# Performance work log

Measured on AMD Instinct MI355X. Metric: run time of the kernel, lower is better.

Reference implementation:

```python
import jax, jax.numpy as jnp
import numpy as np

B = 1024
S_OUT, S_IN, D_IN = 30, 17, 3
H = 4
DKQ_I, DV_I, HID_I, OUT_I = 6, 8, 256, 64
DKQ_O, DV_O, HID_O = 64, 64, 1024
OUT_O = 36 * S_OUT  # 1080


def _mha(x, wq, bq, wk, bk, wv, bv, dkq):
    """Vectorized multi-head self-attention over all heads at once.
    x: [..., P, d_in]; wq/wk: [H, d_in, dkq]; wv: [H, d_in, dv].
    Returns context [..., H, P, dv] (matches torch stack+permute ordering)."""
    q = jnp.einsum('...pd,hdk->...hpk', x, wq) + bq[:, None, :]
    k = jnp.einsum('...pd,hdk->...hpk', x, wk) + bk[:, None, :]
    v = jnp.einsum('...pd,hdv->...hpv', x, wv) + bv[:, None, :]
    scores = jnp.einsum('...hpk,...hqk->...hpq', q, k) / jnp.sqrt(jnp.asarray(dkq, x.dtype))
    attn = jax.nn.softmax(scores, axis=-1)
    return jnp.einsum('...hpq,...hqv->...hpv', attn, v)


def _ml(ctx, w1, b1, w2, b2):
    """MultiHeadLinearLayer: per-head fc1+tanh (shared weights), concat heads, fc2.
    ctx: [..., H, P, dv] -> [..., out]."""
    lead = ctx.shape[:-3]
    flat = ctx.reshape(*lead, H, -1)            # [..., H, P*dv]
    h = jnp.tanh(flat @ w1 + b1)                # [..., H, hidden]
    h = h.reshape(*lead, -1)                    # [..., H*hidden]
    return h @ w2 + b2


def setup_inputs() -> dict:
    key = jax.random.key(0)
    ks = iter(jax.random.split(key, 32))
    n = lambda shape, s=0.05: jax.random.normal(next(ks), shape, dtype=jnp.float32) * s
    inp = {
        'x': jax.random.normal(next(ks), (B, S_OUT, S_IN, D_IN), dtype=jnp.float32),
        # inner multi-head attention (4 heads, stacked weights)
        'iwq': n((H, D_IN, DKQ_I)), 'ibq': n((H, DKQ_I)),
        'iwk': n((H, D_IN, DKQ_I)), 'ibk': n((H, DKQ_I)),
        'iwv': n((H, D_IN, DV_I)),  'ibv': n((H, DV_I)),
        # inner MultiHeadLinearLayer
        'iw1': n((S_IN * DV_I, HID_I)), 'ib1': n((HID_I,)),
        'iw2': n((H * HID_I, OUT_I)),   'ib2': n((OUT_I,)),
        # outer multi-head attention
        'owq': n((H, OUT_I, DKQ_O)), 'obq': n((H, DKQ_O)),
        'owk': n((H, OUT_I, DKQ_O)), 'obk': n((H, DKQ_O)),
        'owv': n((H, OUT_I, DV_O)),  'obv': n((H, DV_O)),
        # outer MultiHeadLinearLayer
        'ow1': n((S_OUT * DV_O, HID_O)), 'ob1': n((HID_O,)),
        'ow2': n((H * HID_O, OUT_O)),    'ob2': n((OUT_O,)),
    }
    return inp


def reference(x, iwq, ibq, iwk, ibk, iwv, ibv, iw1, ib1, iw2, ib2,
              owq, obq, owk, obk, owv, obv, ow1, ob1, ow2, ob2):
    b = x.shape[0]
    # Inner attention applied to all 30 outer positions at once (replaces python loop)
    ctx_i = _mha(x, iwq, ibq, iwk, ibk, iwv, ibv, DKQ_I)      # [B,30,H,17,8]
    seq = _ml(ctx_i, iw1, ib1, iw2, ib2)                       # [B,30,64]
    # Outer attention over the 30-step sequence
    ctx_o = _mha(seq, owq, obq, owk, obk, owv, obv, DKQ_O)     # [B,H,30,64]
    out = _ml(ctx_o, ow1, ob1, ow2, ob2)                       # [B,1080]
    return out.reshape(b, S_OUT, 12, 3)
```

## Files before the change

kernel.cpp:

```cpp
#include <hip/hip_runtime.h>


typedef _Float16 f16x8 __attribute__((ext_vector_type(8)));
typedef _Float16 f16x4 __attribute__((ext_vector_type(4)));
typedef float    f32x4 __attribute__((ext_vector_type(4)));
typedef float    f32x16 __attribute__((ext_vector_type(16)));

union F16x8u { f16x8 v; f16x4 q[2]; };

typedef __attribute__((address_space(1))) const unsigned int as1_u32;
typedef __attribute__((address_space(3))) unsigned int as3_u32;

__device__ inline void gl_lds16(const _Float16* g, _Float16* l) {
    __builtin_amdgcn_global_load_lds((as1_u32*)g, (as3_u32*)l, 16, 0, 0);
}

__device__ inline float tanh_fast(float x) {
    float ax = fabsf(x);
    float e  = __expf(2.0f * ax);
    float r  = 1.0f - 2.0f / (e + 1.0f);
    return copysignf(r, x);
}

__device__ inline f32x16 zero16() {
    f32x16 z;
    #pragma unroll
    for (int i = 0; i < 16; i++) z[i] = 0.f;
    return z;
}

__device__ inline void tcast_tile(
    const float* __restrict__ W, _Float16* __restrict__ Wt,
    int tileIdx, int nkx, int K, int N, int Kpad,
    _Float16 (*tile)[65], int t)
{
    const int kx = tileIdx % nkx, ny = tileIdx / nkx;
    const int k0 = kx * 64, n0 = ny * 64;
    for (int i = t; i < 4096; i += 256) {
        const int r = i >> 6, c = i & 63;
        const int k = k0 + r, n = n0 + c;
        float v = (k < K && n < N) ? W[(size_t)k * N + n] : 0.f;
        tile[c][r] = (_Float16)v;
    }
    __syncthreads();
    for (int i = t; i < 4096; i += 256) {
        const int r = i >> 6, c = i & 63;
        Wt[(size_t)(n0 + r) * Kpad + k0 + c] = tile[r][c];
    }
}

__global__ __launch_bounds__(256) void k_prep_all(
    const float* __restrict__ iwq, const float* __restrict__ ibq,
    const float* __restrict__ iwk, const float* __restrict__ ibk,
    const float* __restrict__ iwv, const float* __restrict__ ibv,
    const float* __restrict__ iw1, const float* __restrict__ iw2,
    const float* __restrict__ ow1, const float* __restrict__ ow2,
    const float* __restrict__ owq, const float* __restrict__ owk,
    const float* __restrict__ owv,
    _Float16* __restrict__ wqf, _Float16* __restrict__ wkf,
    _Float16* __restrict__ wvf,
    _Float16* __restrict__ iw1t, _Float16* __restrict__ iw2t,
    _Float16* __restrict__ ow1t, _Float16* __restrict__ ow2t,
    _Float16* __restrict__ owqt, _Float16* __restrict__ owkt,
    _Float16* __restrict__ owvt)
{
    __shared__ _Float16 tile[64][65];
    const int b = blockIdx.x, t = threadIdx.x;
    if (b == 0) {
        const float SC = 0.40824829046386307f;
        for (int i = t; i < 512; i += 256) {
            const int lanev = i >> 3, jj = i & 7;
            const int n = lanev & 31, grp = lanev >> 5;
            const int h = n >> 3, dk = n & 7;
            float q = 0.f, k = 0.f, v = 0.f;
            if (!grp) {
                if (jj < 3) {
                    if (dk < 6) { q = iwq[h*18 + jj*6 + dk] * SC; k = iwk[h*18 + jj*6 + dk]; }
                    v = iwv[h*24 + jj*8 + dk];
                } else if (jj == 3) {
                    if (dk < 6) { q = ibq[h*6 + dk] * SC; k = ibk[h*6 + dk]; }
                    v = ibv[h*8 + dk];
                }
            }
            wqf[i] = (_Float16)q; wkf[i] = (_Float16)k; wvf[i] = (_Float16)v;
        }
    } else if (b < 161) {
        const int idx = (b - 1) * 256 + t;
        if (idx < 40960) {
            const int n = idx / 160, kp = idx - n * 160;
            const int dv = kp / 20, p = kp - dv * 20;
            float v = (p < 17) ? iw1[(p*8 + dv) * 256 + n] : 0.f;
            iw1t[n * 160 + kp] = (_Float16)v;
        }
    } else if (b < 177) {
        tcast_tile(iw2, iw2t, b - 161, 16, 1024, 64, 1024, tile, t);
    } else if (b < 657) {
        tcast_tile(ow1, ow1t, b - 177, 30, 1920, 1024, 1920, tile, t);
    } else if (b < 1745) {
        tcast_tile(ow2, ow2t, b - 657, 64, 4096, 1080, 4096, tile, t);
    } else {
        const int s = b - 1745;
        const int mat = s >> 6, rem = s & 63;
        const int h = rem >> 4, blk = rem & 15;
        const int idx = blk * 256 + t;
        const int n = idx >> 6, k = idx & 63;
        const float* W = (mat == 0) ? owq : (mat == 1) ? owk : owv;
        _Float16* Wt   = (mat == 0) ? owqt : (mat == 1) ? owkt : owvt;
        Wt[h * 4096 + n * 64 + k] = (_Float16)W[h * 4096 + k * 64 + n];
    }
}

__global__ __launch_bounds__(256, 3) void k_inner_attn_mfma(
    const float* __restrict__ x,
    const _Float16* __restrict__ wqf, const _Float16* __restrict__ wkf,
    const _Float16* __restrict__ wvf,
    _Float16* __restrict__ flat)
{
    __shared__ __align__(16) _Float16 lds[4][5248];
    const int t = threadIdx.x, lane = t & 63, w = t >> 6;
    const int l31 = lane & 31, grp = lane >> 5;
    const int bs = blockIdx.x * 4 + w;
    _Float16* kq  = &lds[w][0];
    _Float16* qq  = &lds[w][1152];
    _Float16* vt  = &lds[w][2304];
    _Float16* pf  = &lds[w][3456];
    _Float16* fo2 = &lds[w][4608];

    f16x8 xf;
    #pragma unroll
    for (int i = 0; i < 8; i++) xf[i] = (_Float16)0.f;
    if (grp == 0 && l31 < 17) {
        const float* xr = x + (size_t)bs * 51 + l31 * 3;
        xf[0] = (_Float16)xr[0];
        xf[1] = (_Float16)xr[1];
        xf[2] = (_Float16)xr[2];
        xf[3] = (_Float16)1.0f;
    }
    const f16x8 wq8 = *(const f16x8*)&wqf[lane * 8];
    const f16x8 wk8 = *(const f16x8*)&wkf[lane * 8];
    const f16x8 wv8 = *(const f16x8*)&wvf[lane * 8];

    f32x16 kt = __builtin_amdgcn_mfma_f32_32x32x16_f16(wk8, xf, zero16(), 0, 0, 0);
    f32x16 qt = __builtin_amdgcn_mfma_f32_32x32x16_f16(wq8, xf, zero16(), 0, 0, 0);
    f32x16 vv = __builtin_amdgcn_mfma_f32_32x32x16_f16(xf, wv8, zero16(), 0, 0, 0);

    #pragma unroll
    for (int qd = 0; qd < 4; qd++) {
        const int base = 8 * qd + 4 * grp;
        f16x4 a, b, c;
        #pragma unroll
        for (int i = 0; i < 4; i++) {
            a[i] = (_Float16)kt[4*qd + i];
            b[i] = (_Float16)qt[4*qd + i];
            c[i] = (_Float16)vv[4*qd + i];
        }
        *(f16x4*)&kq[l31 * 36 + base] = a;
        *(f16x4*)&qq[l31 * 36 + base] = b;
        *(f16x4*)&vt[l31 * 36 + base] = c;
    }

    #pragma unroll
    for (int h = 0; h < 4; h++) {
        F16x8u ka, qb;
        #pragma unroll
        for (int i = 0; i < 8; i++) { ka.v[i] = (_Float16)0.f; qb.v[i] = (_Float16)0.f; }
        if (grp == 0) {
            ka.q[0] = *(const f16x4*)&kq[l31 * 36 + h * 8];
            ka.q[1] = *(const f16x4*)&kq[l31 * 36 + h * 8 + 4];
            qb.q[0] = *(const f16x4*)&qq[l31 * 36 + h * 8];
            qb.q[1] = *(const f16x4*)&qq[l31 * 36 + h * 8 + 4];
        }
        f32x16 s = __builtin_amdgcn_mfma_f32_32x32x16_f16(ka.v, qb.v, zero16(), 0, 0, 0);

        float mx = -1e30f;
        #pragma unroll
        for (int r = 0; r < 16; r++) {
            const bool val = (r < 8) || (r == 8 && grp == 0);
            if (val) mx = fmaxf(mx, s[r]);
        }
        mx = fmaxf(mx, __shfl_xor(mx, 32));
        float e[16], sum = 0.f;
        #pragma unroll
        for (int r = 0; r < 16; r++) {
            const bool val = (r < 8) || (r == 8 && grp == 0);
            e[r] = val ? __expf(s[r] - mx) : 0.f;
            sum += e[r];
        }
        sum += __shfl_xor(sum, 32);
        const float inv = __builtin_amdgcn_rcpf(sum);
        #pragma unroll
        for (int qd = 0; qd < 4; qd++) {
            f16x4 pk;
            #pragma unroll
            for (int i = 0; i < 4; i++) pk[i] = (_Float16)(e[4*qd + i] * inv);
            *(f16x4*)&pf[l31 * 36 + 8 * qd + 4 * grp] = pk;
        }

        F16x8u pa1, pa2, vb1, vb2;
        pa1.q[0] = *(const f16x4*)&pf[l31 * 36 + grp * 8];
        pa1.q[1] = *(const f16x4*)&pf[l31 * 36 + grp * 8 + 4];
        pa2.q[0] = *(const f16x4*)&pf[l31 * 36 + 16 + grp * 8];
        pa2.q[1] = *(const f16x4*)&pf[l31 * 36 + 16 + grp * 8 + 4];
        const int vr = (h * 8 + (l31 & 7)) * 36;
        vb1.q[0] = *(const f16x4*)&vt[vr + grp * 8];
        vb1.q[1] = *(const f16x4*)&vt[vr + grp * 8 + 4];
        vb2.q[0] = *(const f16x4*)&vt[vr + 16 + grp * 8];
        vb2.q[1] = *(const f16x4*)&vt[vr + 16 + grp * 8 + 4];
        f32x16 c = __builtin_amdgcn_mfma_f32_32x32x16_f16(pa1.v, vb1.v, zero16(), 0, 0, 0);
        c = __builtin_amdgcn_mfma_f32_32x32x16_f16(pa2.v, vb2.v, c, 0, 0, 0);

        if (l31 < 8) {
            #pragma unroll
            for (int qd = 0; qd < 4; qd++) {
                const int jb = 8 * qd + 4 * grp;
                if (jb < 20) {
                    f16x4 ck;
                    #pragma unroll
                    for (int i = 0; i < 4; i++) ck[i] = (_Float16)c[4*qd + i];
                    *(f16x4*)&fo2[h * 160 + l31 * 20 + jb] = ck;
                }
            }
        }
    }

    _Float16* fg = flat + (size_t)bs * 640;
    *(f16x8*)&fg[lane * 8] = *(const f16x8*)&fo2[lane * 8];
    if (lane < 16)
        *(f16x8*)&fg[512 + lane * 8] = *(const f16x8*)&fo2[512 + lane * 8];
}

__global__ __launch_bounds__(256) void k_inner_ml_mfma(
    const _Float16* __restrict__ flat,
    const _Float16* __restrict__ iw1t,
    const _Float16* __restrict__ iw2t,
    const float* __restrict__ ib1, const float* __restrict__ ib2,
    float* __restrict__ seq)
{
    __shared__ __align__(16) char ldsbuf[16 * 1032 * 2];
    _Float16* Af = (_Float16*)ldsbuf;
    _Float16 (*h1l)[1032] = (_Float16 (*)[1032])ldsbuf;
    float* red = (float*)ldsbuf;
    const int t = threadIdx.x, lane = t & 63, w = t >> 6;
    const int q = lane >> 4, ml = lane & 15;
    const int m0  = blockIdx.x * 64;
    const int bs0 = blockIdx.x * 16;

    {
        const _Float16* gbase = flat + (size_t)m0 * 160;
        #pragma unroll
        for (int i = 0; i < 5; i++) {
            const int chunk0 = i * 256 + w * 64;
            gl_lds16(gbase + (size_t)(chunk0 + lane) * 8, Af + (size_t)chunk0 * 8);
        }
    }
    __syncthreads();

    f32x4 acc[4][4];
    #pragma unroll
    for (int mi = 0; mi < 4; mi++)
        #pragma unroll
        for (int ni = 0; ni < 4; ni++) acc[mi][ni] = (f32x4){0.f,0.f,0.f,0.f};
    f16x8 bpp[2][4];
    #pragma unroll
    for (int ni = 0; ni < 4; ni++)
        bpp[0][ni] = *(const f16x8*)&iw1t[(size_t)(w*64 + ni*16 + ml) * 160 + q*8];
    #pragma unroll
    for (int ks = 0; ks < 5; ks++) {
        const int cur = ks & 1, nxt = cur ^ 1;
        if (ks < 4) {
            const int kn = (ks + 1) * 32 + q * 8;
            #pragma unroll
            for (int ni = 0; ni < 4; ni++)
                bpp[nxt][ni] = *(const f16x8*)&iw1t[(size_t)(w*64 + ni*16 + ml) * 160 + kn];
        }
        const int k = ks * 32 + q * 8;
        f16x8 a[4];
        #pragma unroll
        for (int mi = 0; mi < 4; mi++)
            a[mi] = *(const f16x8*)&Af[(size_t)(mi*16 + ml) * 160 + k];
        #pragma unroll
        for (int mi = 0; mi < 4; mi++)
            #pragma unroll
            for (int ni = 0; ni < 4; ni++)
                acc[mi][ni] = __builtin_amdgcn_mfma_f32_16x16x32_f16(a[mi], bpp[cur][ni], acc[mi][ni], 0, 0, 0);
    }
    __syncthreads();

    #pragma unroll
    for (int mi = 0; mi < 4; mi++)
        #pragma unroll
        for (int ni = 0; ni < 4; ni++)
            #pragma unroll
            for (int r = 0; r < 4; r++) {
                const int row = mi*16 + q*4 + r;
                const int col = w*64 + ni*16 + ml;
                const int bs_l = row >> 2, h = row & 3;
                h1l[bs_l][h*256 + col] = (_Float16)tanh_fast(acc[mi][ni][r] + ib1[col]);
            }
    __syncthreads();

    f32x4 a2[4];
    #pragma unroll
    for (int ni = 0; ni < 4; ni++) a2[ni] = (f32x4){0.f,0.f,0.f,0.f};
    f16x8 b2[2][4];
    #pragma unroll
    for (int ni = 0; ni < 4; ni++)
        b2[0][ni] = *(const f16x8*)&iw2t[(size_t)(ni*16 + ml) * 1024 + w*256 + q*8];
    #pragma unroll
    for (int ks = 0; ks < 8; ks++) {
        const int cur = ks & 1, nxt = cur ^ 1;
        if (ks < 7) {
            const int kn = w * 256 + (ks + 1) * 32 + q * 8;
            #pragma unroll
            for (int ni = 0; ni < 4; ni++)
                b2[nxt][ni] = *(const f16x8*)&iw2t[(size_t)(ni*16 + ml) * 1024 + kn];
        }
        const int k = w * 256 + ks * 32 + q * 8;
        f16x8 a = *(const f16x8*)&h1l[ml][k];
        #pragma unroll
        for (int ni = 0; ni < 4; ni++)
            a2[ni] = __builtin_amdgcn_mfma_f32_16x16x32_f16(a, b2[cur][ni], a2[ni], 0, 0, 0);
    }
    __syncthreads();
    #pragma unroll
    for (int ni = 0; ni < 4; ni++)
        #pragma unroll
        for (int r = 0; r < 4; r++) {
            const int row = q*4 + r;
            const int col = ni*16 + ml;
            red[(size_t)w*1024 + row*64 + col] = a2[ni][r];
        }
    __syncthreads();
    for (int i = t; i < 1024; i += 256) {
        const int row = i >> 6, col = i & 63;
        float s = red[i] + red[1024 + i] + red[2048 + i] + red[3072 + i] + ib2[col];
        seq[(size_t)(bs0 + row) * 64 + col] = s;
    }
}

__device__ inline void oa_proj_rows(
    const _Float16 (*seqf)[72], const _Float16* __restrict__ wt,
    const float* __restrict__ bias, _Float16 (*dst)[72], int q, int ml)
{
    f32x4 acc[2][4];
    #pragma unroll
    for (int mi = 0; mi < 2; mi++)
        #pragma unroll
        for (int ni = 0; ni < 4; ni++) acc[mi][ni] = (f32x4){0.f,0.f,0.f,0.f};
    #pragma unroll
    for (int k0 = 0; k0 < 64; k0 += 32) {
        f16x8 a[2], bb[4];
        #pragma unroll
        for (int mi = 0; mi < 2; mi++) a[mi] = *(const f16x8*)&seqf[mi*16 + ml][k0 + q*8];
        #pragma unroll
        for (int ni = 0; ni < 4; ni++) bb[ni] = *(const f16x8*)&wt[(size_t)(ni*16 + ml)*64 + k0 + q*8];
        #pragma unroll
        for (int mi = 0; mi < 2; mi++)
            #pragma unroll
            for (int ni = 0; ni < 4; ni++)
                acc[mi][ni] = __builtin_amdgcn_mfma_f32_16x16x32_f16(a[mi], bb[ni], acc[mi][ni], 0, 0, 0);
    }
    #pragma unroll
    for (int ni = 0; ni < 4; ni++) {
        const float bi = bias[ni*16 + ml];
        #pragma unroll
        for (int mi = 0; mi < 2; mi++)
            #pragma unroll
            for (int r = 0; r < 4; r++)
                dst[mi*16 + q*4 + r][ni*16 + ml] = (_Float16)(acc[mi][ni][r] + bi);
    }
}

__device__ inline void oa_proj_t(
    const _Float16 (*seqf)[72], const _Float16* __restrict__ wt,
    const float* __restrict__ bias, _Float16 (*dstT)[40], int q, int ml)
{
    f32x4 acc[2][4];
    #pragma unroll
    for (int mi = 0; mi < 2; mi++)
        #pragma unroll
        for (int ni = 0; ni < 4; ni++) acc[mi][ni] = (f32x4){0.f,0.f,0.f,0.f};
    #pragma unroll
    for (int k0 = 0; k0 < 64; k0 += 32) {
        f16x8 a[2], bb[4];
        #pragma unroll
        for (int mi = 0; mi < 2; mi++) a[mi] = *(const f16x8*)&seqf[mi*16 + ml][k0 + q*8];
        #pragma unroll
        for (int ni = 0; ni < 4; ni++) bb[ni] = *(const f16x8*)&wt[(size_t)(ni*16 + ml)*64 + k0 + q*8];
        #pragma unroll
        for (int mi = 0; mi < 2; mi++)
            #pragma unroll
            for (int ni = 0; ni < 4; ni++)
                acc[mi][ni] = __builtin_amdgcn_mfma_f32_16x16x32_f16(a[mi], bb[ni], acc[mi][ni], 0, 0, 0);
    }
    #pragma unroll
    for (int ni = 0; ni < 4; ni++) {
        const float bi = bias[ni*16 + ml];
        #pragma unroll
        for (int mi = 0; mi < 2; mi++)
            #pragma unroll
            for (int r = 0; r < 4; r++)
                dstT[ni*16 + ml][mi*16 + q*4 + r] = (_Float16)(acc[mi][ni][r] + bi);
    }
}

__global__ __launch_bounds__(256) void k_outer_attn_mfma(
    const float* __restrict__ seq,
    const _Float16* __restrict__ owqt,
    const _Float16* __restrict__ owkt,
    const _Float16* __restrict__ owvt,
    const float* __restrict__ obq, const float* __restrict__ obk,
    const float* __restrict__ obv,
    _Float16* __restrict__ ctxo)
{
    __shared__ __align__(16) _Float16 seqf[32][72];
    __shared__ __align__(16) _Float16 qf[4][32][72];
    __shared__ __align__(16) _Float16 kf[4][32][72];
    __shared__ __align__(16) _Float16 vt[4][64][40];
    __shared__ __align__(16) _Float16 pf[4][32][40];
    const int t = threadIdx.x, lane = t & 63, w = t >> 6;
    const int q = lane >> 4, ml = lane & 15;
    const int b = blockIdx.x;

    const float* sb = seq + (size_t)b * 1920;
    for (int i = t; i < 2048; i += 256) {
        const int row = i >> 6, col = i & 63;
        seqf[row][col] = (_Float16)(row < 30 ? sb[row*64 + col] : 0.0f);
    }
    __syncthreads();

    oa_proj_rows(seqf, owqt + w*4096, obq + w*64, qf[w], q, ml);
    oa_proj_rows(seqf, owkt + w*4096, obk + w*64, kf[w], q, ml);
    oa_proj_t   (seqf, owvt + w*4096, obv + w*64, vt[w], q, ml);
    __syncthreads();

    f32x4 sc[2][2];
    #pragma unroll
    for (int mi = 0; mi < 2; mi++)
        #pragma unroll
        for (int ni = 0; ni < 2; ni++) sc[mi][ni] = (f32x4){0.f,0.f,0.f,0.f};
    #pragma unroll
    for (int k0 = 0; k0 < 64; k0 += 32) {
        f16x8 aq[2], bk[2];
        #pragma unroll
        for (int mi = 0; mi < 2; mi++) aq[mi] = *(const f16x8*)&qf[w][mi*16 + ml][k0 + q*8];
        #pragma unroll
        for (int ni = 0; ni < 2; ni++) bk[ni] = *(const f16x8*)&kf[w][ni*16 + ml][k0 + q*8];
        #pragma unroll
        for (int mi = 0; mi < 2; mi++)
            #pragma unroll
            for (int ni = 0; ni < 2; ni++)
                sc[mi][ni] = __builtin_amdgcn_mfma_f32_16x16x32_f16(aq[mi], bk[ni], sc[mi][ni], 0, 0, 0);
    }

    const bool maskhi = (ml >= 14);
    #pragma unroll
    for (int mi = 0; mi < 2; mi++) {
        #pragma unroll
        for (int r = 0; r < 4; r++) {
            const float s0 = sc[mi][0][r] * 0.125f;
            const float s1 = maskhi ? -1e30f : sc[mi][1][r] * 0.125f;
            float mx = fmaxf(s0, s1);
            #pragma unroll
            for (int off = 1; off < 16; off <<= 1) mx = fmaxf(mx, __shfl_xor(mx, off, 64));
            const float e0 = __expf(s0 - mx);
            const float e1 = __expf(s1 - mx);
            float sm = e0 + e1;
            #pragma unroll
            for (int off = 1; off < 16; off <<= 1) sm += __shfl_xor(sm, off, 64);
            const float inv = 1.0f / sm;
            pf[w][mi*16 + q*4 + r][ml]      = (_Float16)(e0 * inv);
            pf[w][mi*16 + q*4 + r][16 + ml] = (_Float16)(e1 * inv);
        }
    }
    __syncthreads();

    f16x8 ap[2], bv[4];
    #pragma unroll
    for (int mi = 0; mi < 2; mi++) ap[mi] = *(const f16x8*)&pf[w][mi*16 + ml][q*8];
    #pragma unroll
    for (int ni = 0; ni < 4; ni++) bv[ni] = *(const f16x8*)&vt[w][ni*16 + ml][q*8];
    f32x4 oa[2][4];
    #pragma unroll
    for (int mi = 0; mi < 2; mi++)
        #pragma unroll
        for (int ni = 0; ni < 4; ni++) {
            oa[mi][ni] = (f32x4){0.f,0.f,0.f,0.f};
            oa[mi][ni] = __builtin_amdgcn_mfma_f32_16x16x32_f16(ap[mi], bv[ni], oa[mi][ni], 0, 0, 0);
        }

    _Float16* co = ctxo + (size_t)(b*4 + w) * 1920;
    #pragma unroll
    for (int mi = 0; mi < 2; mi++)
        #pragma unroll
        for (int r = 0; r < 4; r++) {
            const int row = mi*16 + q*4 + r;
            if (row < 30) {
                #pragma unroll
                for (int ni = 0; ni < 4; ni++)
                    co[row*64 + ni*16 + ml] = (_Float16)oa[mi][ni][r];
            }
        }
}

__global__ __launch_bounds__(256) void k_outer_fc1_mfma(
    const _Float16* __restrict__ ctxo,
    const _Float16* __restrict__ ow1t,
    const float* __restrict__ ob1,
    _Float16* __restrict__ hout)
{
    __shared__ __align__(16) _Float16 At[128][32];
    __shared__ __align__(16) _Float16 Bt[64][32];
    const int t = threadIdx.x, lane = t & 63, w = t >> 6;
    const int q = lane >> 4, ml = lane & 15;
    const int M0 = (int)(blockIdx.x >> 4) * 128;
    const int N0 = (int)(blockIdx.x & 15) * 64;
    const int wm = (w >> 1) * 64, wn = (w & 1) * 32;

    const int lrow = lane >> 2;
    const int lcol = (lane & 3) * 8;
    const _Float16* gA0 = ctxo + (size_t)(M0 + w*32 + lrow) * 1920 + lcol;
    const _Float16* gA1 = gA0 + (size_t)16 * 1920;
    const _Float16* gB0 = ow1t + (size_t)(N0 + w*16 + lrow) * 1920 + lcol;
    _Float16* lA0 = &At[w*32][0];
    _Float16* lA1 = &At[w*32 + 16][0];
    _Float16* lB0 = &Bt[w*16][0];

    f32x4 acc[4][2];
    #pragma unroll
    for (int mi = 0; mi < 4; mi++)
        #pragma unroll
        for (int ni = 0; ni < 2; ni++) acc[mi][ni] = (f32x4){0.f,0.f,0.f,0.f};

    for (int ks = 0; ks < 60; ks++) {
        const int k0 = ks * 32;
        gl_lds16(gA0 + k0, lA0);
        gl_lds16(gA1 + k0, lA1);
        gl_lds16(gB0 + k0, lB0);
        __syncthreads();
        f16x8 a[4], b[2];
        #pragma unroll
        for (int mi = 0; mi < 4; mi++)
            a[mi] = *(const f16x8*)&At[wm + mi*16 + ml][q*8];
        #pragma unroll
        for (int ni = 0; ni < 2; ni++)
            b[ni] = *(const f16x8*)&Bt[wn + ni*16 + ml][q*8];
        #pragma unroll
        for (int mi = 0; mi < 4; mi++)
            #pragma unroll
            for (int ni = 0; ni < 2; ni++)
                acc[mi][ni] = __builtin_amdgcn_mfma_f32_16x16x32_f16(a[mi], b[ni], acc[mi][ni], 0, 0, 0);
        __syncthreads();
    }

    #pragma unroll
    for (int ni = 0; ni < 2; ni++) {
        const int col = N0 + wn + ni*16 + ml;
        const float bias = ob1[col];
        #pragma unroll
        for (int mi = 0; mi < 4; mi++)
            #pragma unroll
            for (int r = 0; r < 4; r++) {
                const int row = M0 + wm + mi*16 + q*4 + r;
                hout[(size_t)row * 1024 + col] = (_Float16)tanh_fast(acc[mi][ni][r] + bias);
            }
    }
}

__global__ __launch_bounds__(256) void k_outer_fc2_mfma(
    const _Float16* __restrict__ hout,
    const _Float16* __restrict__ ow2t,
    float* __restrict__ part)
{
    __shared__ float red[4][32][65];
    const int t = threadIdx.x, lane = t & 63, w = t >> 6;
    const int q = lane >> 4, ml = lane & 15;
    const int bid = blockIdx.x;
    const int kc = bid & 3;
    const int rest = bid >> 2;
    const int M0 = (rest / 17) * 32;
    const int N0 = (rest % 17) * 64;
    const int kk0 = kc * 1024 + w * 256 + q * 8;
    f32x4 acc[2][4];
    #pragma unroll
    for (int mi = 0; mi < 2; mi++)
        #pragma unroll
        for (int ni = 0; ni < 4; ni++) acc[mi][ni] = (f32x4){0.f,0.f,0.f,0.f};
    f16x8 a[2][2], b[2][4];
    #pragma unroll
    for (int mi = 0; mi < 2; mi++)
        a[0][mi] = *(const f16x8*)&hout[(size_t)(M0 + mi*16 + ml) * 4096 + kk0];
    #pragma unroll
    for (int ni = 0; ni < 4; ni++)
        b[0][ni] = *(const f16x8*)&ow2t[(size_t)(N0 + ni*16 + ml) * 4096 + kk0];
    #pragma unroll
    for (int ks = 0; ks < 8; ks++) {
        const int cur = ks & 1, nxt = cur ^ 1;
        if (ks < 7) {
            const int kn = kk0 + (ks + 1) * 32;
            #pragma unroll
            for (int mi = 0; mi < 2; mi++)
                a[nxt][mi] = *(const f16x8*)&hout[(size_t)(M0 + mi*16 + ml) * 4096 + kn];
            #pragma unroll
            for (int ni = 0; ni < 4; ni++)
                b[nxt][ni] = *(const f16x8*)&ow2t[(size_t)(N0 + ni*16 + ml) * 4096 + kn];
        }
        #pragma unroll
        for (int mi = 0; mi < 2; mi++)
            #pragma unroll
            for (int ni = 0; ni < 4; ni++)
                acc[mi][ni] = __builtin_amdgcn_mfma_f32_16x16x32_f16(a[cur][mi], b[cur][ni], acc[mi][ni], 0, 0, 0);
    }
    #pragma unroll
    for (int mi = 0; mi < 2; mi++)
        #pragma unroll
        for (int ni = 0; ni < 4; ni++)
            #pragma unroll
            for (int r = 0; r < 4; r++)
                red[w][mi*16 + q*4 + r][ni*16 + ml] = acc[mi][ni][r];
    __syncthreads();
    for (int i = t; i < 2048; i += 256) {
        const int row = i >> 6, col = i & 63;
        const int n = N0 + col;
        if (n < 1080) {
            const float s = red[0][row][col] + red[1][row][col] + red[2][row][col] + red[3][row][col];
            part[(size_t)kc * 1105920 + (size_t)(M0 + row) * 1080 + n] = s;
        }
    }
}

__global__ __launch_bounds__(256) void k_fc2_reduce(
    const float* __restrict__ part, const float* __restrict__ ob2,
    float* __restrict__ out)
{
    const int idx = blockIdx.x * 256 + threadIdx.x;
    if (idx >= 1105920) return;
    const int n = idx % 1080;
    out[idx] = part[idx] + part[1105920 + idx] + part[2211840 + idx]
             + part[3317760 + idx] + ob2[n];
}

extern "C" void kernel_launch(void* const* d_in, const int* in_sizes, int n_in,
                              void* d_out, int out_size, void* d_ws, size_t ws_size,
                              hipStream_t stream) {
    const float* x   = (const float*)d_in[0];
    const float* iwq = (const float*)d_in[1];
    const float* ibq = (const float*)d_in[2];
    const float* iwk = (const float*)d_in[3];
    const float* ibk = (const float*)d_in[4];
    const float* iwv = (const float*)d_in[5];
    const float* ibv = (const float*)d_in[6];
    const float* iw1 = (const float*)d_in[7];
    const float* ib1 = (const float*)d_in[8];
    const float* iw2 = (const float*)d_in[9];
    const float* ib2 = (const float*)d_in[10];
    const float* owq = (const float*)d_in[11];
    const float* obq = (const float*)d_in[12];
    const float* owk = (const float*)d_in[13];
    const float* obk = (const float*)d_in[14];
    const float* owv = (const float*)d_in[15];
    const float* obv = (const float*)d_in[16];
    const float* ow1 = (const float*)d_in[17];
    const float* ob1 = (const float*)d_in[18];
    const float* ow2 = (const float*)d_in[19];
    const float* ob2 = (const float*)d_in[20];

    char* ws = (char*)d_ws;
    _Float16* iw1t   = (_Float16*)(ws + 0);
    _Float16* wqf    = (_Float16*)(ws + 98304);
    _Float16* wkf    = (_Float16*)(ws + 99328);
    _Float16* wvf    = (_Float16*)(ws + 100352);
    _Float16* iw2t   = (_Float16*)(ws + 163840);
    _Float16* ow1t   = (_Float16*)(ws + 294912);
    _Float16* ow2t   = (_Float16*)(ws + 4227072);
    _Float16* flat   = (_Float16*)(ws + 13139968);
    float*    seq    = (float*)   (ws + 52461568);
    _Float16* owqt   = (_Float16*)(ws + 60325888);
    _Float16* owkt   = (_Float16*)(ws + 60358656);
    _Float16* owvt   = (_Float16*)(ws + 60391424);
    _Float16* ctxo   = (_Float16*)(ws + 13139968);
    float*    part2  = (float*)   (ws + 13139968);
    _Float16* houtb  = (_Float16*)(ws + 40000000);
    float*    out    = (float*)d_out;

    k_prep_all       <<<dim3(1937), dim3(256), 0, stream>>>(
        iwq, ibq, iwk, ibk, iwv, ibv, iw1, iw2, ow1, ow2, owq, owk, owv,
        wqf, wkf, wvf, iw1t, iw2t, ow1t, ow2t, owqt, owkt, owvt);
    k_inner_attn_mfma<<<dim3(7680), dim3(256), 0, stream>>>(x, wqf, wkf, wvf, flat);
    k_inner_ml_mfma  <<<dim3(1920), dim3(256), 0, stream>>>(flat, iw1t, iw2t, ib1, ib2, seq);
    k_outer_attn_mfma<<<dim3(1024), dim3(256), 0, stream>>>(seq, owqt, owkt, owvt, obq, obk, obv, ctxo);
    k_outer_fc1_mfma <<<dim3(512),  dim3(256), 0, stream>>>(ctxo, ow1t, ob1, houtb);
    k_outer_fc2_mfma <<<dim3(2176), dim3(256), 0, stream>>>(houtb, ow2t, part2);
    k_fc2_reduce     <<<dim3(4320), dim3(256), 0, stream>>>(part2, ob2, out);
}
```

Baseline: 330.7 us.

## Fuse inner attention into inner MLP kernel, keeping context in LDS

Merges the inner multi-head attention kernel into the inner MultiHeadLinear kernel. Each wave now computes attention for 4 sequences in a loop and writes the context straight into the LDS A-tile instead of round-tripping the flat fp16 buffer through global memory. This saves one launch and the global write and read of the flattened context, at the cost of larger LDS use per block, lower occupancy for the attention phase, and serialized per-wave attention work. The barrier after fc1 is dropped because the h1 scratch no longer aliases the A tile.

```diff
diff --git a/kernel.cpp b/kernel.cpp
--- a/kernel.cpp
+++ b/kernel.cpp
@@ -110,147 +110,129 @@
     }
 }
 
-__global__ __launch_bounds__(256, 3) void k_inner_attn_mfma(
+__global__ __launch_bounds__(256) void k_inner_fused(
     const float* __restrict__ x,
     const _Float16* __restrict__ wqf, const _Float16* __restrict__ wkf,
     const _Float16* __restrict__ wvf,
-    _Float16* __restrict__ flat)
-{
-    __shared__ __align__(16) _Float16 lds[4][5248];
-    const int t = threadIdx.x, lane = t & 63, w = t >> 6;
-    const int l31 = lane & 31, grp = lane >> 5;
-    const int bs = blockIdx.x * 4 + w;
-    _Float16* kq  = &lds[w][0];
-    _Float16* qq  = &lds[w][1152];
-    _Float16* vt  = &lds[w][2304];
-    _Float16* pf  = &lds[w][3456];
-    _Float16* fo2 = &lds[w][4608];
-
-    f16x8 xf;
-    #pragma unroll
-    for (int i = 0; i < 8; i++) xf[i] = (_Float16)0.f;
-    if (grp == 0 && l31 < 17) {
-        const float* xr = x + (size_t)bs * 51 + l31 * 3;
-        xf[0] = (_Float16)xr[0];
-        xf[1] = (_Float16)xr[1];
-        xf[2] = (_Float16)xr[2];
-        xf[3] = (_Float16)1.0f;
-    }
-    const f16x8 wq8 = *(const f16x8*)&wqf[lane * 8];
-    const f16x8 wk8 = *(const f16x8*)&wkf[lane * 8];
-    const f16x8 wv8 = *(const f16x8*)&wvf[lane * 8];
-
-    f32x16 kt = __builtin_amdgcn_mfma_f32_32x32x16_f16(wk8, xf, zero16(), 0, 0, 0);
-    f32x16 qt = __builtin_amdgcn_mfma_f32_32x32x16_f16(wq8, xf, zero16(), 0, 0, 0);
-    f32x16 vv = __builtin_amdgcn_mfma_f32_32x32x16_f16(xf, wv8, zero16(), 0, 0, 0);
-
-    #pragma unroll
-    for (int qd = 0; qd < 4; qd++) {
-        const int base = 8 * qd + 4 * grp;
-        f16x4 a, b, c;
-        #pragma unroll
-        for (int i = 0; i < 4; i++) {
-            a[i] = (_Float16)kt[4*qd + i];
-            b[i] = (_Float16)qt[4*qd + i];
-            c[i] = (_Float16)vv[4*qd + i];
-        }
-        *(f16x4*)&kq[l31 * 36 + base] = a;
-        *(f16x4*)&qq[l31 * 36 + base] = b;
-        *(f16x4*)&vt[l31 * 36 + base] = c;
-    }
-
-    #pragma unroll
-    for (int h = 0; h < 4; h++) {
-        F16x8u ka, qb;
-        #pragma unroll
-        for (int i = 0; i < 8; i++) { ka.v[i] = (_Float16)0.f; qb.v[i] = (_Float16)0.f; }
-        if (grp == 0) {
-            ka.q[0] = *(const f16x4*)&kq[l31 * 36 + h * 8];
-            ka.q[1] = *(const f16x4*)&kq[l31 * 36 + h * 8 + 4];
-            qb.q[0] = *(const f16x4*)&qq[l31 * 36 + h * 8];
-            qb.q[1] = *(const f16x4*)&qq[l31 * 36 + h * 8 + 4];
-        }
-        f32x16 s = __builtin_amdgcn_mfma_f32_32x32x16_f16(ka.v, qb.v, zero16(), 0, 0, 0);
-
-        float mx = -1e30f;
-        #pragma unroll
-        for (int r = 0; r < 16; r++) {
-            const bool val = (r < 8) || (r == 8 && grp == 0);
-            if (val) mx = fmaxf(mx, s[r]);
-        }
-        mx = fmaxf(mx, __shfl_xor(mx, 32));
-        float e[16], sum = 0.f;
-        #pragma unroll
-        for (int r = 0; r < 16; r++) {
-            const bool val = (r < 8) || (r == 8 && grp == 0);
-            e[r] = val ? __expf(s[r] - mx) : 0.f;
-            sum += e[r];
-        }
-        sum += __shfl_xor(sum, 32);
-        const float inv = __builtin_amdgcn_rcpf(sum);
-        #pragma unroll
-        for (int qd = 0; qd < 4; qd++) {
-            f16x4 pk;
-            #pragma unroll
-            for (int i = 0; i < 4; i++) pk[i] = (_Float16)(e[4*qd + i] * inv);
-            *(f16x4*)&pf[l31 * 36 + 8 * qd + 4 * grp] = pk;
-        }
-
-        F16x8u pa1, pa2, vb1, vb2;
-        pa1.q[0] = *(const f16x4*)&pf[l31 * 36 + grp * 8];
-        pa1.q[1] = *(const f16x4*)&pf[l31 * 36 + grp * 8 + 4];
-        pa2.q[0] = *(const f16x4*)&pf[l31 * 36 + 16 + grp * 8];
-        pa2.q[1] = *(const f16x4*)&pf[l31 * 36 + 16 + grp * 8 + 4];
-        const int vr = (h * 8 + (l31 & 7)) * 36;
-        vb1.q[0] = *(const f16x4*)&vt[vr + grp * 8];
-        vb1.q[1] = *(const f16x4*)&vt[vr + grp * 8 + 4];
-        vb2.q[0] = *(const f16x4*)&vt[vr + 16 + grp * 8];
-        vb2.q[1] = *(const f16x4*)&vt[vr + 16 + grp * 8 + 4];
-        f32x16 c = __builtin_amdgcn_mfma_f32_32x32x16_f16(pa1.v, vb1.v, zero16(), 0, 0, 0);
-        c = __builtin_amdgcn_mfma_f32_32x32x16_f16(pa2.v, vb2.v, c, 0, 0, 0);
-
-        if (l31 < 8) {
-            #pragma unroll
-            for (int qd = 0; qd < 4; qd++) {
-                const int jb = 8 * qd + 4 * grp;
-                if (jb < 20) {
-                    f16x4 ck;
-                    #pragma unroll
-                    for (int i = 0; i < 4; i++) ck[i] = (_Float16)c[4*qd + i];
-                    *(f16x4*)&fo2[h * 160 + l31 * 20 + jb] = ck;
-                }
-            }
-        }
-    }
-
-    _Float16* fg = flat + (size_t)bs * 640;
-    *(f16x8*)&fg[lane * 8] = *(const f16x8*)&fo2[lane * 8];
-    if (lane < 16)
-        *(f16x8*)&fg[512 + lane * 8] = *(const f16x8*)&fo2[512 + lane * 8];
-}
-
-__global__ __launch_bounds__(256) void k_inner_ml_mfma(
-    const _Float16* __restrict__ flat,
     const _Float16* __restrict__ iw1t,
     const _Float16* __restrict__ iw2t,
     const float* __restrict__ ib1, const float* __restrict__ ib2,
     float* __restrict__ seq)
 {
-    __shared__ __align__(16) char ldsbuf[16 * 1032 * 2];
-    _Float16* Af = (_Float16*)ldsbuf;
-    _Float16 (*h1l)[1032] = (_Float16 (*)[1032])ldsbuf;
-    float* red = (float*)ldsbuf;
+    __shared__ __align__(16) _Float16 At[64 * 160];
+    __shared__ __align__(16) char scratch[36864];
     const int t = threadIdx.x, lane = t & 63, w = t >> 6;
+    const int l31 = lane & 31, grp = lane >> 5;
     const int q = lane >> 4, ml = lane & 15;
-    const int m0  = blockIdx.x * 64;
     const int bs0 = blockIdx.x * 16;
 
-    {
-        const _Float16* gbase = flat + (size_t)m0 * 160;
-        #pragma unroll
-        for (int i = 0; i < 5; i++) {
-            const int chunk0 = i * 256 + w * 64;
-            gl_lds16(gbase + (size_t)(chunk0 + lane) * 8, Af + (size_t)chunk0 * 8);
+    _Float16* kq = (_Float16*)scratch + (size_t)w * 4608;
+    _Float16* qq = kq + 1152;
+    _Float16* vt = qq + 1152;
+    _Float16* pf = vt + 1152;
+    _Float16 (*h1l)[1032] = (_Float16 (*)[1032])scratch;
+    float* red = (float*)scratch;
+
+    const f16x8 wq8 = *(const f16x8*)&wqf[lane * 8];
+    const f16x8 wk8 = *(const f16x8*)&wkf[lane * 8];
+    const f16x8 wv8 = *(const f16x8*)&wvf[lane * 8];
+
+    for (int si = 0; si < 4; si++) {
+        const int s_local = w * 4 + si;
+        const int bs = bs0 + s_local;
+
+        f16x8 xf;
+        #pragma unroll
+        for (int i = 0; i < 8; i++) xf[i] = (_Float16)0.f;
+        if (grp == 0 && l31 < 17) {
+            const float* xr = x + (size_t)bs * 51 + l31 * 3;
+            xf[0] = (_Float16)xr[0];
+            xf[1] = (_Float16)xr[1];
+            xf[2] = (_Float16)xr[2];
+            xf[3] = (_Float16)1.0f;
+        }
+        f32x16 kt = __builtin_amdgcn_mfma_f32_32x32x16_f16(wk8, xf, zero16(), 0, 0, 0);
+        f32x16 qt = __builtin_amdgcn_mfma_f32_32x32x16_f16(wq8, xf, zero16(), 0, 0, 0);
+        f32x16 vv = __builtin_amdgcn_mfma_f32_32x32x16_f16(xf, wv8, zero16(), 0, 0, 0);
+
+        #pragma unroll
+        for (int qd = 0; qd < 4; qd++) {
+            const int base = 8 * qd + 4 * grp;
+            f16x4 a, b, c;
+            #pragma unroll
+            for (int i = 0; i < 4; i++) {
+                a[i] = (_Float16)kt[4*qd + i];
+                b[i] = (_Float16)qt[4*qd + i];
+                c[i] = (_Float16)vv[4*qd + i];
+            }
+            *(f16x4*)&kq[l31 * 36 + base] = a;
+            *(f16x4*)&qq[l31 * 36 + base] = b;
+            *(f16x4*)&vt[l31 * 36 + base] = c;
+        }
+
+        #pragma unroll
+        for (int h = 0; h < 4; h++) {
+            F16x8u ka, qb;
+            #pragma unroll
+            for (int i = 0; i < 8; i++) { ka.v[i] = (_Float16)0.f; qb.v[i] = (_Float16)0.f; }
+            if (grp == 0) {
+                ka.q[0] = *(const f16x4*)&kq[l31 * 36 + h * 8];
+                ka.q[1] = *(const f16x4*)&kq[l31 * 36 + h * 8 + 4];
+                qb.q[0] = *(const f16x4*)&qq[l31 * 36 + h * 8];
+                qb.q[1] = *(const f16x4*)&qq[l31 * 36 + h * 8 + 4];
+            }
+            f32x16 s = __builtin_amdgcn_mfma_f32_32x32x16_f16(ka.v, qb.v, zero16(), 0, 0, 0);
+
+            float mx = -1e30f;
+            #pragma unroll
+            for (int r = 0; r < 16; r++) {
+                const bool val = (r < 8) || (r == 8 && grp == 0);
+                if (val) mx = fmaxf(mx, s[r]);
+            }
+            mx = fmaxf(mx, __shfl_xor(mx, 32));
+            float e[16], sum = 0.f;
+            #pragma unroll
+            for (int r = 0; r < 16; r++) {
+                const bool val = (r < 8) || (r == 8 && grp == 0);
+                e[r] = val ? __expf(s[r] - mx) : 0.f;
+                sum += e[r];
+            }
+            sum += __shfl_xor(sum, 32);
+            const float inv = __builtin_amdgcn_rcpf(sum);
+            #pragma unroll
+            for (int qd = 0; qd < 4; qd++) {
+                f16x4 pk;
+                #pragma unroll
+                for (int i = 0; i < 4; i++) pk[i] = (_Float16)(e[4*qd + i] * inv);
+                *(f16x4*)&pf[l31 * 36 + 8 * qd + 4 * grp] = pk;
+            }
+
+            F16x8u pa1, pa2, vb1, vb2;
+            pa1.q[0] = *(const f16x4*)&pf[l31 * 36 + grp * 8];
+            pa1.q[1] = *(const f16x4*)&pf[l31 * 36 + grp * 8 + 4];
+            pa2.q[0] = *(const f16x4*)&pf[l31 * 36 + 16 + grp * 8];
+            pa2.q[1] = *(const f16x4*)&pf[l31 * 36 + 16 + grp * 8 + 4];
+            const int vr = (h * 8 + (l31 & 7)) * 36;
+            vb1.q[0] = *(const f16x4*)&vt[vr + grp * 8];
+            vb1.q[1] = *(const f16x4*)&vt[vr + grp * 8 + 4];
+            vb2.q[0] = *(const f16x4*)&vt[vr + 16 + grp * 8];
+            vb2.q[1] = *(const f16x4*)&vt[vr + 16 + grp * 8 + 4];
+            f32x16 c = __builtin_amdgcn_mfma_f32_32x32x16_f16(pa1.v, vb1.v, zero16(), 0, 0, 0);
+            c = __builtin_amdgcn_mfma_f32_32x32x16_f16(pa2.v, vb2.v, c, 0, 0, 0);
+
+            if (l31 < 8) {
+                _Float16* arow = At + (size_t)(s_local * 4 + h) * 160 + l31 * 20;
+                #pragma unroll
+                for (int qd = 0; qd < 4; qd++) {
+                    const int jb = 8 * qd + 4 * grp;
+                    if (jb < 20) {
+                        f16x4 ck;
+                        #pragma unroll
+                        for (int i = 0; i < 4; i++) ck[i] = (_Float16)c[4*qd + i];
+                        *(f16x4*)&arow[jb] = ck;
+                    }
+                }
+            }
         }
     }
     __syncthreads();
@@ -277,15 +259,13 @@
         f16x8 a[4];
         #pragma unroll
         for (int mi = 0; mi < 4; mi++)
-            a[mi] = *(const f16x8*)&Af[(size_t)(mi*16 + ml) * 160 + k];
+            a[mi] = *(const f16x8*)&At[(size_t)(mi*16 + ml) * 160 + k];
         #pragma unroll
         for (int mi = 0; mi < 4; mi++)
             #pragma unroll
             for (int ni = 0; ni < 4; ni++)
                 acc[mi][ni] = __builtin_amdgcn_mfma_f32_16x16x32_f16(a[mi], bpp[cur][ni], acc[mi][ni], 0, 0, 0);
     }
-    __syncthreads();
-
     #pragma unroll
     for (int mi = 0; mi < 4; mi++)
         #pragma unroll
@@ -673,7 +653,6 @@
     _Float16* iw2t   = (_Float16*)(ws + 163840);
     _Float16* ow1t   = (_Float16*)(ws + 294912);
     _Float16* ow2t   = (_Float16*)(ws + 4227072);
-    _Float16* flat   = (_Float16*)(ws + 13139968);
     float*    seq    = (float*)   (ws + 52461568);
     _Float16* owqt   = (_Float16*)(ws + 60325888);
     _Float16* owkt   = (_Float16*)(ws + 60358656);
@@ -686,8 +665,8 @@
     k_prep_all       <<<dim3(1937), dim3(256), 0, stream>>>(
         iwq, ibq, iwk, ibk, iwv, ibv, iw1, iw2, ow1, ow2, owq, owk, owv,
         wqf, wkf, wvf, iw1t, iw2t, ow1t, ow2t, owqt, owkt, owvt);
-    k_inner_attn_mfma<<<dim3(7680), dim3(256), 0, stream>>>(x, wqf, wkf, wvf, flat);
-    k_inner_ml_mfma  <<<dim3(1920), dim3(256), 0, stream>>>(flat, iw1t, iw2t, ib1, ib2, seq);
+    k_inner_fused    <<<dim3(1920), dim3(256), 0, stream>>>(
+        x, wqf, wkf, wvf, iw1t, iw2t, ib1, ib2, seq);
     k_outer_attn_mfma<<<dim3(1024), dim3(256), 0, stream>>>(seq, owqt, owkt, owvt, obq, obk, obv, ctxo);
     k_outer_fc1_mfma <<<dim3(512),  dim3(256), 0, stream>>>(ctxo, ow1t, ob1, houtb);
     k_outer_fc2_mfma <<<dim3(2176), dim3(256), 0, stream>>>(houtb, ow2t, part2);
```

Measured after the change: 331.2 us. Within noise of the previous version (+0.2%).
